# Optimization experiments

Measured on AMD Instinct MI355X. Metric: run time of the kernel, lower is better.

## Reference

```python
import jax, jax.numpy as jnp
import numpy as np

QBITS = 8  # all quant points configured to 8-bit symmetric by default


def fake_quant(v, bits=QBITS):
    """Symmetric per-tensor fake quantize/dequantize with STE-compatible form."""
    qmax = float(2 ** (bits - 1) - 1)
    scale = jnp.maximum(jnp.max(jnp.abs(v)) / qmax, 1e-8)
    q = jnp.clip(jnp.round(v / scale), -qmax - 1.0, qmax) * scale
    # straight-through estimator (identity gradient)
    return v + jax.lax.stop_gradient(q - v)


def reorder_pt_to_haste(w):
    # PyTorch gate order (r,z,n) -> Haste order (z,r,n) along leading 3H axis
    h3 = w.shape[0] // 3
    return jnp.concatenate([w[h3:2 * h3], w[:h3], w[2 * h3:]], axis=0)


def setup_inputs() -> dict:
    key = jax.random.key(0)
    ks = jax.random.split(key, 6)
    T, B, I, H = 1024, 64, 256, 256
    s = 1.0 / np.sqrt(H)
    return {
        "x": jax.random.normal(ks[0], (T, B, I), dtype=jnp.float32),
        "weight_ih": jax.random.normal(ks[1], (3 * H, I), dtype=jnp.float32) * s,
        "weight_hh": jax.random.normal(ks[2], (3 * H, H), dtype=jnp.float32) * s,
        "bias_ih": jax.random.normal(ks[3], (3 * H,), dtype=jnp.float32) * s,
        "bias_hh": jax.random.normal(ks[4], (3 * H,), dtype=jnp.float32) * s,
        "h0": jax.random.normal(ks[5], (B, H), dtype=jnp.float32),
    }


def _quant_gru(x, weight_ih, weight_hh, bias_ih, bias_hh, h0):
    T, B, I = x.shape
    H = weight_hh.shape[1]
    # Haste layout: W [I,3H], R [H,3H], gate order (z,r,n)
    W = reorder_pt_to_haste(weight_ih).T   # [I, 3H]
    R = reorder_pt_to_haste(weight_hh).T   # [H, 3H]
    bx = reorder_pt_to_haste(bias_ih)      # [3H]
    br = reorder_pt_to_haste(bias_hh)      # [3H]

    # per-tensor fake quant of inputs / weights / biases
    xq = fake_quant(x)
    Wq = fake_quant(W)
    Rq = fake_quant(R)
    bxq = fake_quant(bx)
    brq = fake_quant(br)

    # precompute Wx for all timesteps: [T,B,3H], quantized matmul output
    Wx = fake_quant(jnp.einsum('tbi,ih->tbh', xq, Wq))

    bx_z, bx_r, bx_n = bxq[:H], bxq[H:2 * H], bxq[2 * H:]
    br_z, br_r, br_n = brq[:H], brq[H:2 * H], brq[2 * H:]

    def step(h, wx_t):
        hq = fake_quant(h)
        Rh = fake_quant(hq @ Rq)           # [B, 3H]
        Rh_z, Rh_r, Rh_n = Rh[:, :H], Rh[:, H:2 * H], Rh[:, 2 * H:]
        wx_z, wx_r, wx_n = wx_t[:, :H], wx_t[:, H:2 * H], wx_t[:, 2 * H:]

        z_pre = fake_quant(wx_z + bx_z + Rh_z + br_z)
        z = fake_quant(jax.nn.sigmoid(z_pre))
        r_pre = fake_quant(wx_r + bx_r + Rh_r + br_r)
        r = fake_quant(jax.nn.sigmoid(r_pre))

        Rh_add_br = fake_quant(Rh_n + br_n)
        rRh = fake_quant(r * Rh_add_br)
        g_pre = fake_quant(wx_n + bx_n + rRh)
        g = fake_quant(jnp.tanh(g_pre))

        old_contrib = fake_quant(z * h)
        new_contrib = fake_quant((1.0 - z) * g)
        h_new = old_contrib + new_contrib
        return h_new, h_new

    h_last, output = jax.lax.scan(step, h0, Wx)  # output: [T, B, H]
    return output, h_last[None]  # h_n: [1, B, H]


def reference(x, weight_ih, weight_hh, bias_ih, bias_hh, h0):
    return _quant_gru(x, weight_ih, weight_hh, bias_ih, bias_hh, h0)
```

## Files before the change

### kernel.cpp

```cpp
#include <hip/hip_runtime.h>
#include <cstdint>
#include <cstddef>


typedef int   v4i __attribute__((ext_vector_type(4)));
typedef float v4f __attribute__((ext_vector_type(4)));

#define T_STEPS 1024
#define OUT_MAIN_FLOATS (1024*64*256)
#define WXQ_DOUT_OFF 16842752
#define NWG 8

__device__ __forceinline__ float clamp128(float x) {
  return fminf(fmaxf(x, -128.0f), 127.0f);
}
__device__ __forceinline__ int permj(int j) {
  return j < 256 ? j + 256 : (j < 512 ? j - 256 : j);
}
__device__ __forceinline__ float sigmoidf_(float x) {
  return __fdividef(1.0f, 1.0f + __expf(-x));
}
__device__ __forceinline__ float tanhf_(float x) {
  float e = __expf(-2.0f * fabsf(x));
  float t = __fdividef(1.0f - e, 1.0f + e);
  return copysignf(t, x);
}
__device__ __forceinline__ unsigned skey(float x) {
  unsigned u = __float_as_uint(x);
  return (u & 0x80000000u) ? ~u : (u | 0x80000000u);
}
__device__ __forceinline__ float sdec(unsigned k) {
  unsigned u = (k & 0x80000000u) ? (k ^ 0x80000000u) : ~k;
  return __uint_as_float(u);
}
__device__ __forceinline__ float wave_amax(float v) {
  #pragma unroll
  for (int m = 1; m <= 32; m <<= 1) v = fmaxf(v, __shfl_xor(v, m, 64));
  return v;
}

__device__ __forceinline__ unsigned dpp_wave_max(unsigned v) {
  unsigned t;
  t = (unsigned)__builtin_amdgcn_update_dpp(0, (int)v, 0x111, 0xf, 0xf, true);
  v = v > t ? v : t;
  t = (unsigned)__builtin_amdgcn_update_dpp(0, (int)v, 0x112, 0xf, 0xf, true);
  v = v > t ? v : t;
  t = (unsigned)__builtin_amdgcn_update_dpp(0, (int)v, 0x114, 0xf, 0xf, true);
  v = v > t ? v : t;
  t = (unsigned)__builtin_amdgcn_update_dpp(0, (int)v, 0x118, 0xf, 0xf, true);
  v = v > t ? v : t;
  t = (unsigned)__builtin_amdgcn_update_dpp(0, (int)v, 0x142, 0xf, 0xf, true);
  v = v > t ? v : t;
  t = (unsigned)__builtin_amdgcn_update_dpp(0, (int)v, 0x143, 0xf, 0xf, true);
  v = v > t ? v : t;
  return v;
}

__device__ __forceinline__ void bar_lgkm() {
  asm volatile("s_waitcnt lgkmcnt(0)\n\ts_barrier" ::: "memory");
  __builtin_amdgcn_sched_barrier(0);
}

__device__ __forceinline__ int poll_burst(const unsigned long long* p,
                                          unsigned tag, unsigned* val) {
  unsigned out;
  int fnd;
  unsigned long long scr;
  asm volatile(
    "s_mov_b32 %[fnd], 0\n\t"
    "global_load_dwordx2 v[80:81], %[p], off sc1\n\t"
    "global_load_dwordx2 v[82:83], %[p], off sc0 sc1\n\t"
    "global_load_dwordx2 v[84:85], %[p], off sc1\n\t"
    "global_load_dwordx2 v[86:87], %[p], off sc0 sc1\n\t"

    "s_waitcnt vmcnt(3)\n\t"
    "v_cmp_eq_u32 vcc, %[tg], v81\n\t"
    "s_xor_b64 %[scr], vcc, exec\n\t"
    "s_cbranch_scc0 F0_%=\n\t"
    "global_load_dwordx2 v[80:81], %[p], off sc1\n\t"
    "s_waitcnt vmcnt(3)\n\t"
    "v_cmp_eq_u32 vcc, %[tg], v83\n\t"
    "s_xor_b64 %[scr], vcc, exec\n\t"
    "s_cbranch_scc0 F1_%=\n\t"
    "global_load_dwordx2 v[82:83], %[p], off sc0 sc1\n\t"
    "s_waitcnt vmcnt(3)\n\t"
    "v_cmp_eq_u32 vcc, %[tg], v85\n\t"
    "s_xor_b64 %[scr], vcc, exec\n\t"
    "s_cbranch_scc0 F2_%=\n\t"
    "global_load_dwordx2 v[84:85], %[p], off sc1\n\t"
    "s_waitcnt vmcnt(3)\n\t"
    "v_cmp_eq_u32 vcc, %[tg], v87\n\t"
    "s_xor_b64 %[scr], vcc, exec\n\t"
    "s_cbranch_scc0 F3_%=\n\t"
    "global_load_dwordx2 v[86:87], %[p], off sc0 sc1\n\t"

    "s_waitcnt vmcnt(3)\n\t"
    "v_cmp_eq_u32 vcc, %[tg], v81\n\t"
    "s_xor_b64 %[scr], vcc, exec\n\t"
    "s_cbranch_scc0 F0_%=\n\t"
    "global_load_dwordx2 v[80:81], %[p], off sc1\n\t"
    "s_waitcnt vmcnt(3)\n\t"
    "v_cmp_eq_u32 vcc, %[tg], v83\n\t"
    "s_xor_b64 %[scr], vcc, exec\n\t"
    "s_cbranch_scc0 F1_%=\n\t"
    "global_load_dwordx2 v[82:83], %[p], off sc0 sc1\n\t"
    "s_waitcnt vmcnt(3)\n\t"
    "v_cmp_eq_u32 vcc, %[tg], v85\n\t"
    "s_xor_b64 %[scr], vcc, exec\n\t"
    "s_cbranch_scc0 F2_%=\n\t"
    "global_load_dwordx2 v[84:85], %[p], off sc1\n\t"
    "s_waitcnt vmcnt(3)\n\t"
    "v_cmp_eq_u32 vcc, %[tg], v87\n\t"
    "s_xor_b64 %[scr], vcc, exec\n\t"
    "s_cbranch_scc0 F3_%=\n\t"
    "global_load_dwordx2 v[86:87], %[p], off sc0 sc1\n\t"

    "s_waitcnt vmcnt(3)\n\t"
    "v_cmp_eq_u32 vcc, %[tg], v81\n\t"
    "s_xor_b64 %[scr], vcc, exec\n\t"
    "s_cbranch_scc0 F0_%=\n\t"
    "s_waitcnt vmcnt(2)\n\t"
    "v_cmp_eq_u32 vcc, %[tg], v83\n\t"
    "s_xor_b64 %[scr], vcc, exec\n\t"
    "s_cbranch_scc0 F1_%=\n\t"
    "s_waitcnt vmcnt(1)\n\t"
    "v_cmp_eq_u32 vcc, %[tg], v85\n\t"
    "s_xor_b64 %[scr], vcc, exec\n\t"
    "s_cbranch_scc0 F2_%=\n\t"
    "s_waitcnt vmcnt(0)\n\t"
    "v_cmp_eq_u32 vcc, %[tg], v87\n\t"
    "s_xor_b64 %[scr], vcc, exec\n\t"
    "s_cbranch_scc0 F3_%=\n\t"
    "v_mov_b32 %[out], 0\n\t"
    "s_branch DN_%=\n\t"

    "F0_%=:\n\t"
    "v_mov_b32 %[out], v80\n\t"
    "s_mov_b32 %[fnd], 1\n\t"
    "s_branch DN_%=\n\t"
    "F1_%=:\n\t"
    "v_mov_b32 %[out], v82\n\t"
    "s_mov_b32 %[fnd], 1\n\t"
    "s_branch DN_%=\n\t"
    "F2_%=:\n\t"
    "v_mov_b32 %[out], v84\n\t"
    "s_mov_b32 %[fnd], 1\n\t"
    "s_branch DN_%=\n\t"
    "F3_%=:\n\t"
    "v_mov_b32 %[out], v86\n\t"
    "s_mov_b32 %[fnd], 1\n\t"
    "DN_%=:\n\t"
    "s_waitcnt vmcnt(0)"
    : [out]"=&v"(out), [fnd]"=&s"(fnd), [scr]"=&s"(scr)
    : [p]"v"(p), [tg]"v"(tag)
    : "vcc", "scc", "memory",
      "v80","v81","v82","v83","v84","v85","v86","v87");
  *val = out;
  return fnd;
}

#define MFMA_I8(a, b, c) __builtin_amdgcn_mfma_i32_16x16x64_i8(a, b, c, 0, 0, 0)

__global__ void k_absmax(const float* __restrict__ p, int n4, unsigned* slot) {
  int i = blockIdx.x * blockDim.x + threadIdx.x;
  int stride = gridDim.x * blockDim.x;
  const v4f* p4 = (const v4f*)p;
  float m = 0.0f;
  for (; i < n4; i += stride) {
    v4f v = p4[i];
    m = fmaxf(m, fmaxf(fmaxf(fabsf(v[0]), fabsf(v[1])),
                       fmaxf(fabsf(v[2]), fabsf(v[3]))));
  }
  m = wave_amax(m);
  if ((threadIdx.x & 63) == 0) atomicMax(slot, __float_as_uint(m));
}

__global__ void k_frag(const float* __restrict__ src,
                       const unsigned* __restrict__ slots, int slot_idx,
                       signed char* __restrict__ dst) {
  int id = blockIdx.x * 256 + threadIdx.x;
  float s = fmaxf(__uint_as_float(slots[slot_idx]) / 127.0f, 1e-8f);
  int bq   = id & 3;
  int lane = (id >> 2) & 63;
  int kc   = (id >> 8) & 3;
  int ct   = id >> 10;
  int n = ct * 16 + (lane & 15);
  int k = kc * 64 + (lane >> 4) * 16 + bq * 4;
  const float* p = src + permj(n) * 256 + k;
  int b0 = ((int)clamp128(rintf(p[0] / s))) & 255;
  int b1 = ((int)clamp128(rintf(p[1] / s))) & 255;
  int b2 = ((int)clamp128(rintf(p[2] / s))) & 255;
  int b3 = ((int)clamp128(rintf(p[3] / s))) & 255;
  ((int*)dst)[id] = b0 | (b1 << 8) | (b2 << 16) | (b3 << 24);
}

__global__ void k_bias(const float* __restrict__ bih, const float* __restrict__ bhh,
                       const unsigned* __restrict__ slots, float* __restrict__ bqo) {
  int j = threadIdx.x;
  float s_bx = fmaxf(__uint_as_float(slots[3]) / 127.0f, 1e-8f);
  float s_br = fmaxf(__uint_as_float(slots[4]) / 127.0f, 1e-8f);
  int pr = permj(j);
  bqo[j]       = s_bx * clamp128(rintf(bih[pr] / s_bx));
  bqo[768 + j] = s_br * clamp128(rintf(bhh[pr] / s_br));
}

__global__ void k_xq(const float* __restrict__ x, const unsigned* __restrict__ slots,
                     signed char* __restrict__ xq8, int n4) {
  int i = blockIdx.x * blockDim.x + threadIdx.x;
  if (i >= n4) return;
  float s_x = fmaxf(__uint_as_float(slots[0]) / 127.0f, 1e-8f);
  v4f v = ((const v4f*)x)[i];
  int b0 = ((int)clamp128(rintf(v[0] / s_x))) & 255;
  int b1 = ((int)clamp128(rintf(v[1] / s_x))) & 255;
  int b2 = ((int)clamp128(rintf(v[2] / s_x))) & 255;
  int b3 = ((int)clamp128(rintf(v[3] / s_x))) & 255;
  ((int*)xq8)[i] = b0 | (b1 << 8) | (b2 << 16) | (b3 << 24);
}

__global__ __launch_bounds__(1024) void k_wx_i8(
    const signed char* __restrict__ xq8, const signed char* __restrict__ wf,
    unsigned* __restrict__ slots, signed char* __restrict__ wxq, int mode) {
  const int t = blockIdx.x;
  const int tid = threadIdx.x, lane = tid & 63, w = tid >> 6;
  const int cl = lane & 15, lh = lane >> 4;

  v4i Bz[4], Br[4], Bn[4];
  #pragma unroll
  for (int kc = 0; kc < 4; ++kc) {
    Bz[kc] = *(const v4i*)(wf + (((w)*4      + kc) * 64 + lane) * 16);
    Br[kc] = *(const v4i*)(wf + (((w + 16)*4 + kc) * 64 + lane) * 16);
    Bn[kc] = *(const v4i*)(wf + (((w + 32)*4 + kc) * 64 + lane) * 16);
  }
  v4i acc[3][4];
  #pragma unroll
  for (int p = 0; p < 3; ++p)
    #pragma unroll
    for (int rt = 0; rt < 4; ++rt) acc[p][rt] = (v4i){0, 0, 0, 0};

  const signed char* xr = xq8 + t * 16384;
  #pragma unroll
  for (int kc = 0; kc < 4; ++kc)
    #pragma unroll
    for (int rt = 0; rt < 4; ++rt) {
      v4i A = *(const v4i*)(xr + (rt * 16 + cl) * 256 + kc * 64 + lh * 16);
      acc[0][rt] = MFMA_I8(A, Bz[kc], acc[0][rt]);
      acc[1][rt] = MFMA_I8(A, Br[kc], acc[1][rt]);
      acc[2][rt] = MFMA_I8(A, Bn[kc], acc[2][rt]);
    }

  if (mode == 0) {
    int mm = 0;
    #pragma unroll
    for (int p = 0; p < 3; ++p)
      #pragma unroll
      for (int rt = 0; rt < 4; ++rt)
        #pragma unroll
        for (int rg = 0; rg < 4; ++rg) mm = max(mm, abs(acc[p][rt][rg]));
    #pragma unroll
    for (int m = 1; m <= 32; m <<= 1) mm = max(mm, __shfl_xor(mm, m, 64));
    if (lane == 0) atomicMax((int*)(slots + 5), mm);
  } else {
    int islot = *(const int*)(slots + 5);
    float maxMf = (float)islot;
    float s_x = fmaxf(__uint_as_float(slots[0]) / 127.0f, 1e-8f);
    float s_W = fmaxf(__uint_as_float(slots[1]) / 127.0f, 1e-8f);
    float s_xW = s_x * s_W;
    float s_wx = fmaxf(s_xW * maxMf / 127.0f, 1e-8f);
    #pragma unroll
    for (int p = 0; p < 3; ++p)
      #pragma unroll
      for (int rt = 0; rt < 4; ++rt) {
        int dw = 0;
        #pragma unroll
        for (int rg = 0; rg < 4; ++rg) {
          float qf = clamp128(rintf((s_xW * (float)acc[p][rt][rg]) / s_wx));
          dw |= (((int)qf) & 255) << (rg * 8);
        }
        ((int*)wxq)[t * 12288 + p * 4096 + rt * 1024 + w * 64 + lh * 16 + cl] = dw;
      }
  }
}

template <int NCH>
__device__ __forceinline__ void xchg(unsigned* keys, unsigned tag,
    unsigned (*lred)[8], unsigned long long* gslot, int wg, int tid, int lane) {
  const int rset = tag % 3;
  #pragma unroll
  for (int c = 0; c < NCH; ++c) keys[c] = dpp_wave_max(keys[c]);
  if (lane == 63) {
    #pragma unroll
    for (int c = 0; c < NCH; ++c) atomicMax(&lred[rset][c], keys[c]);
  }
  bar_lgkm();
  const int par = tag & 1;
  if (tid < NCH) {
    unsigned long long v =
        ((unsigned long long)tag << 32) | (unsigned long long)lred[rset][tid];
    __hip_atomic_store(&gslot[(par * NWG + wg) * 8 + tid], v,
                       __ATOMIC_RELAXED, __HIP_MEMORY_SCOPE_AGENT);
  } else if (tid == 32) {
    int ns = rset + 1; if (ns == 3) ns = 0;
    #pragma unroll
    for (int c = 0; c < 8; ++c) lred[ns][c] = 0u;
  } else if (tid >= 64 && tid < 64 + (NWG - 1) * NCH) {
    int idx = tid - 64;
    int owi = idx / NCH;
    int c = idx - owi * NCH;
    int ow = owi + (owi >= wg ? 1 : 0);
    unsigned long long* p = &gslot[(par * NWG + ow) * 8 + c];
    unsigned val;
    for (;;) {
      if (poll_burst(p, tag, &val)) break;
      unsigned long long v =
          __hip_atomic_load(p, __ATOMIC_RELAXED, __HIP_MEMORY_SCOPE_AGENT);
      if ((unsigned)(v >> 32) == tag) { val = (unsigned)v; break; }
    }
    atomicMax(&lred[rset][c], val);
  }
  bar_lgkm();
  #pragma unroll
  for (int c = 0; c < NCH; ++c) keys[c] = lred[rset][c];
}

__global__ __launch_bounds__(512, 1) void k_recur8(
    const signed char* __restrict__ wxq, const signed char* __restrict__ brf,
    const float* __restrict__ bq, const unsigned* __restrict__ slots,
    const float* __restrict__ h0p, float* __restrict__ out,
    unsigned long long* __restrict__ gslot) {
  __shared__ signed char ah[16 * 272];
  __shared__ int zs[8 * 256];
  __shared__ int rs_[8 * 256];
  __shared__ int ns_[8 * 256];
  __shared__ unsigned lred[3][8];

  const int tid = threadIdx.x;
  const int lane = tid & 63;
  const int w = tid >> 6;
  const int cl = lane & 15;
  const int lh = lane >> 4;
  const int wg = blockIdx.x;
  const int j = tid & 255;
  const int rblk = tid >> 8;

  if (tid < 24) ((unsigned*)lred)[tid] = 0u;
  for (int i = tid; i < 1088; i += 512) ((int*)ah)[i] = 0;

  float s_x = fmaxf(__uint_as_float(slots[0]) / 127.0f, 1e-8f);
  float s_W = fmaxf(__uint_as_float(slots[1]) / 127.0f, 1e-8f);
  float s_R = fmaxf(__uint_as_float(slots[2]) / 127.0f, 1e-8f);
  float maxM0 = (float)(*(const int*)(slots + 5));
  float s_wx = fmaxf(s_x * s_W * maxM0 / 127.0f, 1e-8f);

  float bxz = bq[j], bxr = bq[j + 256], bxn = bq[j + 512];
  float brz = bq[768 + j], brr = bq[1024 + j], brn = bq[1280 + j];

  v4i Bz[2][4], Br[2][4], Bn[2][4];
  #pragma unroll
  for (int cg = 0; cg < 2; ++cg) {
    int ct = w * 2 + cg;
    #pragma unroll
    for (int kc = 0; kc < 4; ++kc) {
      Bz[cg][kc] = *(const v4i*)(brf + ((ct * 4        + kc) * 64 + lane) * 16);
      Br[cg][kc] = *(const v4i*)(brf + (((ct + 16) * 4 + kc) * 64 + lane) * 16);
      Bn[cg][kc] = *(const v4i*)(brf + (((ct + 32) * 4 + kc) * 64 + lane) * 16);
    }
  }

  float h[4];
  #pragma unroll
  for (int rg = 0; rg < 4; ++rg)
    h[rg] = h0p[(wg * 8 + rblk * 4 + rg) * 256 + j];

  __syncthreads();

  unsigned tag = 1;
  float sh;
  {
    float m = fmaxf(fmaxf(fabsf(h[0]), fabsf(h[1])),
                    fmaxf(fabsf(h[2]), fabsf(h[3])));
    unsigned kk[1] = {__float_as_uint(m)};
    xchg<1>(kk, tag++, lred, gslot, wg, tid, lane);
    sh = fmaxf(__uint_as_float(kk[0]) / 127.0f, 1e-8f);
    float ish = 1.0f / sh;
    #pragma unroll
    for (int rg = 0; rg < 4; ++rg)
      ah[(rblk * 4 + rg) * 272 + j] = (signed char)(int)rintf(h[rg] * ish);
    bar_lgkm();
  }

  const int rt_ = wg >> 1;
  const int lhb = ((wg & 1) << 1) | rblk;
  const int widx0 = rt_ * 1024 + (j >> 4) * 64 + lhb * 16 + (j & 15);

  for (int t = 0; t < T_STEPS; ++t) {
    const int* wxi = (const int*)wxq + (size_t)t * 12288 + widx0;
    int wvz = wxi[0];
    int wvr = wxi[4096];
    int wvn = wxi[8192];

    v4i aZ[2] = {(v4i){0,0,0,0}, (v4i){0,0,0,0}};
    v4i aR[2] = {(v4i){0,0,0,0}, (v4i){0,0,0,0}};
    v4i aN[2] = {(v4i){0,0,0,0}, (v4i){0,0,0,0}};
    #pragma unroll
    for (int kc = 0; kc < 4; ++kc) {
      v4i A = *(const v4i*)(ah + cl * 272 + kc * 64 + lh * 16);
      #pragma unroll
      for (int cg = 0; cg < 2; ++cg) {
        aZ[cg] = MFMA_I8(A, Bz[cg][kc], aZ[cg]);
        aR[cg] = MFMA_I8(A, Br[cg][kc], aR[cg]);
        aN[cg] = MFMA_I8(A, Bn[cg][kc], aN[cg]);
      }
    }

    if (lane < 32) {
      #pragma unroll
      for (int cg = 0; cg < 2; ++cg) {
        int jj = (w * 2 + cg) * 16 + cl;
        #pragma unroll
        for (int rg = 0; rg < 4; ++rg) {
          int row = lh * 4 + rg;
          zs[row * 256 + jj] = aZ[cg][rg];
          rs_[row * 256 + jj] = aR[cg][rg];
          ns_[row * 256 + jj] = aN[cg][rg];
        }
      }
    }

    int mm = 0;
    #pragma unroll
    for (int cg = 0; cg < 2; ++cg)
      #pragma unroll
      for (int rg = 0; rg < 4; ++rg)
        mm = max(mm, max(abs(aZ[cg][rg]),
                         max(abs(aR[cg][rg]), abs(aN[cg][rg]))));
    unsigned kk[5];
    kk[0] = (unsigned)mm;
    xchg<1>(kk, tag++, lred, gslot, wg, tid, lane);
    float maxMf = (float)(int)kk[0];
    float s_Rh = fmaxf(sh * s_R * maxMf / 127.0f, 1e-8f);
    float fRh = (sh * s_R) / s_Rh;

    float zp[4], rp[4], nb[4];
    float az = 0.0f, ar = 0.0f, an = 0.0f;
    float mzs = -3.402823466e38f, mrs = -3.402823466e38f;
    #pragma unroll
    for (int rg = 0; rg < 4; ++rg) {
      int row = rblk * 4 + rg;
      float Rz = s_Rh * rintf((float)zs[row * 256 + j] * fRh);
      float Rr = s_Rh * rintf((float)rs_[row * 256 + j] * fRh);
      float Rn = s_Rh * rintf((float)ns_[row * 256 + j] * fRh);
      float wz = s_wx * (float)((signed char)(wvz >> (rg * 8)));
      float wr = s_wx * (float)((signed char)(wvr >> (rg * 8)));
      float a1 = ((wz + bxz) + Rz) + brz;
      float a2 = ((wr + bxr) + Rr) + brr;
      float a3 = Rn + brn;
      zp[rg] = a1; rp[rg] = a2; nb[rg] = a3;
      az = fmaxf(az, fabsf(a1)); ar = fmaxf(ar, fabsf(a2));
      an = fmaxf(an, fabsf(a3));
      mzs = fmaxf(mzs, a1); mrs = fmaxf(mrs, a2);
    }
    kk[0] = __float_as_uint(az); kk[1] = __float_as_uint(ar);
    kk[2] = __float_as_uint(an); kk[3] = skey(mzs); kk[4] = skey(mrs);
    xchg<5>(kk, tag++, lred, gslot, wg, tid, lane);
    float s1 = fmaxf(__uint_as_float(kk[0]) / 127.0f, 1e-8f), i1 = 1.0f / s1;
    float s2 = fmaxf(__uint_as_float(kk[1]) / 127.0f, 1e-8f), i2 = 1.0f / s2;
    float s3 = fmaxf(__uint_as_float(kk[2]) / 127.0f, 1e-8f), i3 = 1.0f / s3;
    float zq_max = s1 * rintf(sdec(kk[3]) * i1);
    float rq_max = s2 * rintf(sdec(kk[4]) * i2);
    float s4 = fmaxf(sigmoidf_(zq_max) / 127.0f, 1e-8f), i4 = 1.0f / s4;
    float s5 = fmaxf(sigmoidf_(rq_max) / 127.0f, 1e-8f), i5 = 1.0f / s5;

    float zf[4], rr_[4];
    float m6 = 0.0f;
    #pragma unroll
    for (int rg = 0; rg < 4; ++rg) {
      float zq = s1 * rintf(zp[rg] * i1);
      float rq = s2 * rintf(rp[rg] * i2);
      float zv = sigmoidf_(zq);
      float rv = sigmoidf_(rq);
      zf[rg] = s4 * rintf(zv * i4);
      float rq2 = s5 * rintf(rv * i5);
      float nbq = s3 * rintf(nb[rg] * i3);
      float rr = rq2 * nbq;
      rr_[rg] = rr;
      m6 = fmaxf(m6, fabsf(rr));
    }
    kk[0] = __float_as_uint(m6);
    xchg<1>(kk, tag++, lred, gslot, wg, tid, lane);
    float s6 = fmaxf(__uint_as_float(kk[0]) / 127.0f, 1e-8f), i6 = 1.0f / s6;

    float gp[4];
    float m7 = 0.0f;
    #pragma unroll
    for (int rg = 0; rg < 4; ++rg) {
      float rrq = s6 * rintf(rr_[rg] * i6);
      float wn = s_wx * (float)((signed char)(wvn >> (rg * 8)));
      float g = (wn + bxn) + rrq;
      gp[rg] = g;
      m7 = fmaxf(m7, fabsf(g));
    }
    kk[0] = __float_as_uint(m7);
    xchg<1>(kk, tag++, lred, gslot, wg, tid, lane);
    float m7g = __uint_as_float(kk[0]);
    float s7 = fmaxf(m7g / 127.0f, 1e-8f), i7 = 1.0f / s7;
    float gq_max = s7 * rintf(m7g * i7);
    float s8 = fmaxf(tanhf_(gq_max) / 127.0f, 1e-8f), i8v = 1.0f / s8;

    float ov[4], nv[4];
    float mo = 0.0f, mn = 0.0f;
    #pragma unroll
    for (int rg = 0; rg < 4; ++rg) {
      float gpq = s7 * rintf(gp[rg] * i7);
      float gv = tanhf_(gpq);
      float gq = s8 * rintf(gv * i8v);
      float o = zf[rg] * h[rg];
      float n = (1.0f - zf[rg]) * gq;
      ov[rg] = o; nv[rg] = n;
      mo = fmaxf(mo, fabsf(o)); mn = fmaxf(mn, fabsf(n));
    }
    kk[0] = __float_as_uint(mo); kk[1] = __float_as_uint(mn);
    xchg<2>(kk, tag++, lred, gslot, wg, tid, lane);
    float s9  = fmaxf(__uint_as_float(kk[0]) / 127.0f, 1e-8f), i9  = 1.0f / s9;
    float s10 = fmaxf(__uint_as_float(kk[1]) / 127.0f, 1e-8f), i10 = 1.0f / s10;

    float mh = 0.0f;
    #pragma unroll
    for (int rg = 0; rg < 4; ++rg) {
      float oq = s9  * rintf(ov[rg] * i9);
      float nq = s10 * rintf(nv[rg] * i10);
      float hn = oq + nq;
      h[rg] = hn;
      mh = fmaxf(mh, fabsf(hn));
      out[t * 16384 + (wg * 8 + rblk * 4 + rg) * 256 + j] = hn;
    }
    kk[0] = __float_as_uint(mh);
    xchg<1>(kk, tag++, lred, gslot, wg, tid, lane);
    sh = fmaxf(__uint_as_float(kk[0]) / 127.0f, 1e-8f);
    float ish = 1.0f / sh;
    #pragma unroll
    for (int rg = 0; rg < 4; ++rg)
      ah[(rblk * 4 + rg) * 272 + j] = (signed char)(int)rintf(h[rg] * ish);
    bar_lgkm();
  }

  #pragma unroll
  for (int rg = 0; rg < 4; ++rg)
    out[OUT_MAIN_FLOATS + (wg * 8 + rblk * 4 + rg) * 256 + j] = h[rg];
}

extern "C" void kernel_launch(void* const* d_in, const int* in_sizes, int n_in,
                              void* d_out, int out_size, void* d_ws, size_t ws_size,
                              hipStream_t stream) {
  const float* x   = (const float*)d_in[0];
  const float* wih = (const float*)d_in[1];
  const float* whh = (const float*)d_in[2];
  const float* bih = (const float*)d_in[3];
  const float* bhh = (const float*)d_in[4];
  const float* h0  = (const float*)d_in[5];
  float* out = (float*)d_out;

  unsigned* slots = (unsigned*)d_ws;
  unsigned long long* gslot = (unsigned long long*)((char*)d_ws + 512);
  float* bq       = (float*)((char*)d_ws + 4096);
  signed char* F  = (signed char*)d_ws + 10240;

  signed char* wxq = (signed char*)d_out + WXQ_DOUT_OFF;
  signed char* xq8 = (signed char*)d_out;

  hipMemsetAsync(d_ws, 0, 4096, stream);

  k_absmax<<<dim3(1024), dim3(256), 0, stream>>>(x,   16777216 / 4, slots + 0);
  k_absmax<<<dim3(96),   dim3(256), 0, stream>>>(wih, 196608 / 4,   slots + 1);
  k_absmax<<<dim3(96),   dim3(256), 0, stream>>>(whh, 196608 / 4,   slots + 2);
  k_absmax<<<dim3(1),    dim3(256), 0, stream>>>(bih, 768 / 4,      slots + 3);
  k_absmax<<<dim3(1),    dim3(256), 0, stream>>>(bhh, 768 / 4,      slots + 4);

  k_frag<<<dim3(192), dim3(256), 0, stream>>>(wih, slots, 1, F);
  k_bias<<<dim3(1), dim3(768), 0, stream>>>(bih, bhh, slots, bq);
  k_xq<<<dim3(16384), dim3(256), 0, stream>>>(x, slots, xq8, 4194304);

  k_wx_i8<<<dim3(1024), dim3(1024), 0, stream>>>(xq8, F, slots, wxq, 0);
  k_wx_i8<<<dim3(1024), dim3(1024), 0, stream>>>(xq8, F, slots, wxq, 1);

  k_frag<<<dim3(192), dim3(256), 0, stream>>>(whh, slots, 2, F);

  k_recur8<<<dim3(NWG), dim3(512), 0, stream>>>(wxq, F, bq, slots, h0, out,
                                                gslot);
}
```

Before: 12.70 ms.

## Replace first block barrier in cross-workgroup max exchange with last-arriver counter

```diff
diff --git a/kernel.cpp b/kernel.cpp
--- a/kernel.cpp
+++ b/kernel.cpp
@@ -283,26 +283,42 @@
 
 template <int NCH>
 __device__ __forceinline__ void xchg(unsigned* keys, unsigned tag,
-    unsigned (*lred)[8], unsigned long long* gslot, int wg, int tid, int lane) {
+    unsigned (*lred)[8], unsigned* lredw, unsigned* cnt,
+    unsigned long long* gslot, int wg, int tid, int lane, int w) {
   const int rset = tag % 3;
+  const int par = tag & 1;
   #pragma unroll
   for (int c = 0; c < NCH; ++c) keys[c] = dpp_wave_max(keys[c]);
+  int old = -1;
   if (lane == 63) {
     #pragma unroll
-    for (int c = 0; c < NCH; ++c) atomicMax(&lred[rset][c], keys[c]);
-  }
-  bar_lgkm();
-  const int par = tag & 1;
-  if (tid < NCH) {
-    unsigned long long v =
-        ((unsigned long long)tag << 32) | (unsigned long long)lred[rset][tid];
-    __hip_atomic_store(&gslot[(par * NWG + wg) * 8 + tid], v,
-                       __ATOMIC_RELAXED, __HIP_MEMORY_SCOPE_AGENT);
-  } else if (tid == 32) {
+    for (int c = 0; c < NCH; ++c) lredw[c * 8 + w] = keys[c];
+    asm volatile("s_waitcnt lgkmcnt(0)" ::: "memory");
+    old = (int)atomicAdd(&cnt[rset], 1u);
+  }
+  if (old == 7) {
+    #pragma unroll
+    for (int c = 0; c < NCH; ++c) {
+      unsigned M = lredw[c * 8 + 0];
+      #pragma unroll
+      for (int ww = 1; ww < 8; ++ww) {
+        unsigned t2 = lredw[c * 8 + ww];
+        M = M > t2 ? M : t2;
+      }
+      unsigned long long v =
+          ((unsigned long long)tag << 32) | (unsigned long long)M;
+      __hip_atomic_store(&gslot[(par * NWG + wg) * 8 + c], v,
+                         __ATOMIC_RELAXED, __HIP_MEMORY_SCOPE_AGENT);
+      atomicMax(&lred[rset][c], M);
+    }
+  }
+  if (tid == 32) {
     int ns = rset + 1; if (ns == 3) ns = 0;
     #pragma unroll
     for (int c = 0; c < 8; ++c) lred[ns][c] = 0u;
-  } else if (tid >= 64 && tid < 64 + (NWG - 1) * NCH) {
+    cnt[ns] = 0u;
+  }
+  if (tid >= 64 && tid < 64 + (NWG - 1) * NCH) {
     int idx = tid - 64;
     int owi = idx / NCH;
     int c = idx - owi * NCH;
@@ -332,6 +348,8 @@
   __shared__ int rs_[8 * 256];
   __shared__ int ns_[8 * 256];
   __shared__ unsigned lred[3][8];
+  __shared__ unsigned lredw[64];
+  __shared__ unsigned cnt[3];
 
   const int tid = threadIdx.x;
   const int lane = tid & 63;
@@ -343,6 +361,7 @@
   const int rblk = tid >> 8;
 
   if (tid < 24) ((unsigned*)lred)[tid] = 0u;
+  if (tid >= 24 && tid < 27) cnt[tid - 24] = 0u;
   for (int i = tid; i < 1088; i += 512) ((int*)ah)[i] = 0;
 
   float s_x = fmaxf(__uint_as_float(slots[0]) / 127.0f, 1e-8f);
@@ -379,7 +398,7 @@
     float m = fmaxf(fmaxf(fabsf(h[0]), fabsf(h[1])),
                     fmaxf(fabsf(h[2]), fabsf(h[3])));
     unsigned kk[1] = {__float_as_uint(m)};
-    xchg<1>(kk, tag++, lred, gslot, wg, tid, lane);
+    xchg<1>(kk, tag++, lred, lredw, cnt, gslot, wg, tid, lane, w);
     sh = fmaxf(__uint_as_float(kk[0]) / 127.0f, 1e-8f);
     float ish = 1.0f / sh;
     #pragma unroll
@@ -435,7 +454,7 @@
                          max(abs(aR[cg][rg]), abs(aN[cg][rg]))));
     unsigned kk[5];
     kk[0] = (unsigned)mm;
-    xchg<1>(kk, tag++, lred, gslot, wg, tid, lane);
+    xchg<1>(kk, tag++, lred, lredw, cnt, gslot, wg, tid, lane, w);
     float maxMf = (float)(int)kk[0];
     float s_Rh = fmaxf(sh * s_R * maxMf / 127.0f, 1e-8f);
     float fRh = (sh * s_R) / s_Rh;
@@ -461,7 +480,7 @@
     }
     kk[0] = __float_as_uint(az); kk[1] = __float_as_uint(ar);
     kk[2] = __float_as_uint(an); kk[3] = skey(mzs); kk[4] = skey(mrs);
-    xchg<5>(kk, tag++, lred, gslot, wg, tid, lane);
+    xchg<5>(kk, tag++, lred, lredw, cnt, gslot, wg, tid, lane, w);
     float s1 = fmaxf(__uint_as_float(kk[0]) / 127.0f, 1e-8f), i1 = 1.0f / s1;
     float s2 = fmaxf(__uint_as_float(kk[1]) / 127.0f, 1e-8f), i2 = 1.0f / s2;
     float s3 = fmaxf(__uint_as_float(kk[2]) / 127.0f, 1e-8f), i3 = 1.0f / s3;
@@ -486,7 +505,7 @@
       m6 = fmaxf(m6, fabsf(rr));
     }
     kk[0] = __float_as_uint(m6);
-    xchg<1>(kk, tag++, lred, gslot, wg, tid, lane);
+    xchg<1>(kk, tag++, lred, lredw, cnt, gslot, wg, tid, lane, w);
     float s6 = fmaxf(__uint_as_float(kk[0]) / 127.0f, 1e-8f), i6 = 1.0f / s6;
 
     float gp[4];
@@ -500,7 +519,7 @@
       m7 = fmaxf(m7, fabsf(g));
     }
     kk[0] = __float_as_uint(m7);
-    xchg<1>(kk, tag++, lred, gslot, wg, tid, lane);
+    xchg<1>(kk, tag++, lred, lredw, cnt, gslot, wg, tid, lane, w);
     float m7g = __uint_as_float(kk[0]);
     float s7 = fmaxf(m7g / 127.0f, 1e-8f), i7 = 1.0f / s7;
     float gq_max = s7 * rintf(m7g * i7);
@@ -519,7 +538,7 @@
       mo = fmaxf(mo, fabsf(o)); mn = fmaxf(mn, fabsf(n));
     }
     kk[0] = __float_as_uint(mo); kk[1] = __float_as_uint(mn);
-    xchg<2>(kk, tag++, lred, gslot, wg, tid, lane);
+    xchg<2>(kk, tag++, lred, lredw, cnt, gslot, wg, tid, lane, w);
     float s9  = fmaxf(__uint_as_float(kk[0]) / 127.0f, 1e-8f), i9  = 1.0f / s9;
     float s10 = fmaxf(__uint_as_float(kk[1]) / 127.0f, 1e-8f), i10 = 1.0f / s10;
 
@@ -534,7 +553,7 @@
       out[t * 16384 + (wg * 8 + rblk * 4 + rg) * 256 + j] = hn;
     }
     kk[0] = __float_as_uint(mh);
-    xchg<1>(kk, tag++, lred, gslot, wg, tid, lane);
+    xchg<1>(kk, tag++, lred, lredw, cnt, gslot, wg, tid, lane, w);
     sh = fmaxf(__uint_as_float(kk[0]) / 127.0f, 1e-8f);
     float ish = 1.0f / sh;
     #pragma unroll
```

After: 14.09 ms. +11.0%, slower.

## Double recurrence block to 1024 threads, one MFMA column tile per wave

Applied to the files above, without the earlier changes.

```diff
diff --git a/kernel.cpp b/kernel.cpp
--- a/kernel.cpp
+++ b/kernel.cpp
@@ -322,7 +322,7 @@
   for (int c = 0; c < NCH; ++c) keys[c] = lred[rset][c];
 }
 
-__global__ __launch_bounds__(512, 1) void k_recur8(
+__global__ __launch_bounds__(1024, 1) void k_recur8(
     const signed char* __restrict__ wxq, const signed char* __restrict__ brf,
     const float* __restrict__ bq, const unsigned* __restrict__ slots,
     const float* __restrict__ h0p, float* __restrict__ out,
@@ -343,7 +343,7 @@
   const int rblk = tid >> 8;
 
   if (tid < 24) ((unsigned*)lred)[tid] = 0u;
-  for (int i = tid; i < 1088; i += 512) ((int*)ah)[i] = 0;
+  for (int i = tid; i < 1088; i += 1024) ((int*)ah)[i] = 0;
 
   float s_x = fmaxf(__uint_as_float(slots[0]) / 127.0f, 1e-8f);
   float s_W = fmaxf(__uint_as_float(slots[1]) / 127.0f, 1e-8f);
@@ -354,43 +354,39 @@
   float bxz = bq[j], bxr = bq[j + 256], bxn = bq[j + 512];
   float brz = bq[768 + j], brr = bq[1024 + j], brn = bq[1280 + j];
 
-  v4i Bz[2][4], Br[2][4], Bn[2][4];
-  #pragma unroll
-  for (int cg = 0; cg < 2; ++cg) {
-    int ct = w * 2 + cg;
-    #pragma unroll
-    for (int kc = 0; kc < 4; ++kc) {
-      Bz[cg][kc] = *(const v4i*)(brf + ((ct * 4        + kc) * 64 + lane) * 16);
-      Br[cg][kc] = *(const v4i*)(brf + (((ct + 16) * 4 + kc) * 64 + lane) * 16);
-      Bn[cg][kc] = *(const v4i*)(brf + (((ct + 32) * 4 + kc) * 64 + lane) * 16);
-    }
-  }
-
-  float h[4];
-  #pragma unroll
-  for (int rg = 0; rg < 4; ++rg)
-    h[rg] = h0p[(wg * 8 + rblk * 4 + rg) * 256 + j];
+  v4i Bz[4], Br[4], Bn[4];
+  #pragma unroll
+  for (int kc = 0; kc < 4; ++kc) {
+    Bz[kc] = *(const v4i*)(brf + ((w * 4        + kc) * 64 + lane) * 16);
+    Br[kc] = *(const v4i*)(brf + (((w + 16) * 4 + kc) * 64 + lane) * 16);
+    Bn[kc] = *(const v4i*)(brf + (((w + 32) * 4 + kc) * 64 + lane) * 16);
+  }
+
+  float h[2];
+  #pragma unroll
+  for (int s = 0; s < 2; ++s)
+    h[s] = h0p[(wg * 8 + rblk * 2 + s) * 256 + j];
 
   __syncthreads();
 
   unsigned tag = 1;
   float sh;
   {
-    float m = fmaxf(fmaxf(fabsf(h[0]), fabsf(h[1])),
-                    fmaxf(fabsf(h[2]), fabsf(h[3])));
+    float m = fmaxf(fabsf(h[0]), fabsf(h[1]));
     unsigned kk[1] = {__float_as_uint(m)};
     xchg<1>(kk, tag++, lred, gslot, wg, tid, lane);
     sh = fmaxf(__uint_as_float(kk[0]) / 127.0f, 1e-8f);
     float ish = 1.0f / sh;
     #pragma unroll
-    for (int rg = 0; rg < 4; ++rg)
-      ah[(rblk * 4 + rg) * 272 + j] = (signed char)(int)rintf(h[rg] * ish);
+    for (int s = 0; s < 2; ++s)
+      ah[(rblk * 2 + s) * 272 + j] = (signed char)(int)rintf(h[s] * ish);
     bar_lgkm();
   }
 
-  const int rt_ = wg >> 1;
-  const int lhb = ((wg & 1) << 1) | rblk;
-  const int widx0 = rt_ * 1024 + (j >> 4) * 64 + lhb * 16 + (j & 15);
+  const int widx0 = (wg >> 1) * 1024 +
+                    (((wg << 1) | (rblk >> 1)) & 3) * 16 +
+                    (j >> 4) * 64 + (j & 15);
+  const int bb = (rblk & 1) * 2;
 
   for (int t = 0; t < T_STEPS; ++t) {
     const int* wxi = (const int*)wxq + (size_t)t * 12288 + widx0;
@@ -398,41 +394,30 @@
     int wvr = wxi[4096];
     int wvn = wxi[8192];
 
-    v4i aZ[2] = {(v4i){0,0,0,0}, (v4i){0,0,0,0}};
-    v4i aR[2] = {(v4i){0,0,0,0}, (v4i){0,0,0,0}};
-    v4i aN[2] = {(v4i){0,0,0,0}, (v4i){0,0,0,0}};
+    v4i aZ = {0,0,0,0}, aR = {0,0,0,0}, aN = {0,0,0,0};
     #pragma unroll
     for (int kc = 0; kc < 4; ++kc) {
       v4i A = *(const v4i*)(ah + cl * 272 + kc * 64 + lh * 16);
+      aZ = MFMA_I8(A, Bz[kc], aZ);
+      aR = MFMA_I8(A, Br[kc], aR);
+      aN = MFMA_I8(A, Bn[kc], aN);
+    }
+
+    if (lane < 32) {
+      int jj = w * 16 + cl;
       #pragma unroll
-      for (int cg = 0; cg < 2; ++cg) {
-        aZ[cg] = MFMA_I8(A, Bz[cg][kc], aZ[cg]);
-        aR[cg] = MFMA_I8(A, Br[cg][kc], aR[cg]);
-        aN[cg] = MFMA_I8(A, Bn[cg][kc], aN[cg]);
+      for (int rg = 0; rg < 4; ++rg) {
+        int row = lh * 4 + rg;
+        zs[row * 256 + jj] = aZ[rg];
+        rs_[row * 256 + jj] = aR[rg];
+        ns_[row * 256 + jj] = aN[rg];
       }
     }
 
-    if (lane < 32) {
-      #pragma unroll
-      for (int cg = 0; cg < 2; ++cg) {
-        int jj = (w * 2 + cg) * 16 + cl;
-        #pragma unroll
-        for (int rg = 0; rg < 4; ++rg) {
-          int row = lh * 4 + rg;
-          zs[row * 256 + jj] = aZ[cg][rg];
-          rs_[row * 256 + jj] = aR[cg][rg];
-          ns_[row * 256 + jj] = aN[cg][rg];
-        }
-      }
-    }
-
     int mm = 0;
     #pragma unroll
-    for (int cg = 0; cg < 2; ++cg)
-      #pragma unroll
-      for (int rg = 0; rg < 4; ++rg)
-        mm = max(mm, max(abs(aZ[cg][rg]),
-                         max(abs(aR[cg][rg]), abs(aN[cg][rg]))));
+    for (int rg = 0; rg < 4; ++rg)
+      mm = max(mm, max(abs(aZ[rg]), max(abs(aR[rg]), abs(aN[rg]))));
     unsigned kk[5];
     kk[0] = (unsigned)mm;
     xchg<1>(kk, tag++, lred, gslot, wg, tid, lane);
@@ -440,21 +425,21 @@
     float s_Rh = fmaxf(sh * s_R * maxMf / 127.0f, 1e-8f);
     float fRh = (sh * s_R) / s_Rh;
 
-    float zp[4], rp[4], nb[4];
+    float zp[2], rp[2], nb[2];
     float az = 0.0f, ar = 0.0f, an = 0.0f;
     float mzs = -3.402823466e38f, mrs = -3.402823466e38f;
     #pragma unroll
-    for (int rg = 0; rg < 4; ++rg) {
-      int row = rblk * 4 + rg;
+    for (int s = 0; s < 2; ++s) {
+      int row = rblk * 2 + s;
       float Rz = s_Rh * rintf((float)zs[row * 256 + j] * fRh);
       float Rr = s_Rh * rintf((float)rs_[row * 256 + j] * fRh);
       float Rn = s_Rh * rintf((float)ns_[row * 256 + j] * fRh);
-      float wz = s_wx * (float)((signed char)(wvz >> (rg * 8)));
-      float wr = s_wx * (float)((signed char)(wvr >> (rg * 8)));
+      float wz = s_wx * (float)((signed char)(wvz >> ((bb + s) * 8)));
+      float wr = s_wx * (float)((signed char)(wvr >> ((bb + s) * 8)));
       float a1 = ((wz + bxz) + Rz) + brz;
       float a2 = ((wr + bxr) + Rr) + brr;
       float a3 = Rn + brn;
-      zp[rg] = a1; rp[rg] = a2; nb[rg] = a3;
+      zp[s] = a1; rp[s] = a2; nb[s] = a3;
       az = fmaxf(az, fabsf(a1)); ar = fmaxf(ar, fabsf(a2));
       an = fmaxf(an, fabsf(a3));
       mzs = fmaxf(mzs, a1); mrs = fmaxf(mrs, a2);
@@ -470,33 +455,33 @@
     float s4 = fmaxf(sigmoidf_(zq_max) / 127.0f, 1e-8f), i4 = 1.0f / s4;
     float s5 = fmaxf(sigmoidf_(rq_max) / 127.0f, 1e-8f), i5 = 1.0f / s5;
 
-    float zf[4], rr_[4];
+    float zf[2], rr_[2];
     float m6 = 0.0f;
     #pragma unroll
-    for (int rg = 0; rg < 4; ++rg) {
-      float zq = s1 * rintf(zp[rg] * i1);
-      float rq = s2 * rintf(rp[rg] * i2);
+    for (int s = 0; s < 2; ++s) {
+      float zq = s1 * rintf(zp[s] * i1);
+      float rq = s2 * rintf(rp[s] * i2);
       float zv = sigmoidf_(zq);
       float rv = sigmoidf_(rq);
-      zf[rg] = s4 * rintf(zv * i4);
+      zf[s] = s4 * rintf(zv * i4);
       float rq2 = s5 * rintf(rv * i5);
-      float nbq = s3 * rintf(nb[rg] * i3);
+      float nbq = s3 * rintf(nb[s] * i3);
       float rr = rq2 * nbq;
-      rr_[rg] = rr;
+      rr_[s] = rr;
       m6 = fmaxf(m6, fabsf(rr));
     }
     kk[0] = __float_as_uint(m6);
     xchg<1>(kk, tag++, lred, gslot, wg, tid, lane);
     float s6 = fmaxf(__uint_as_float(kk[0]) / 127.0f, 1e-8f), i6 = 1.0f / s6;
 
-    float gp[4];
+    float gp[2];
     float m7 = 0.0f;
     #pragma unroll
-    for (int rg = 0; rg < 4; ++rg) {
-      float rrq = s6 * rintf(rr_[rg] * i6);
-      float wn = s_wx * (float)((signed char)(wvn >> (rg * 8)));
+    for (int s = 0; s < 2; ++s) {
+      float rrq = s6 * rintf(rr_[s] * i6);
+      float wn = s_wx * (float)((signed char)(wvn >> ((bb + s) * 8)));
       float g = (wn + bxn) + rrq;
-      gp[rg] = g;
+      gp[s] = g;
       m7 = fmaxf(m7, fabsf(g));
     }
     kk[0] = __float_as_uint(m7);
@@ -506,16 +491,16 @@
     float gq_max = s7 * rintf(m7g * i7);
     float s8 = fmaxf(tanhf_(gq_max) / 127.0f, 1e-8f), i8v = 1.0f / s8;
 
-    float ov[4], nv[4];
+    float ov[2], nv[2];
     float mo = 0.0f, mn = 0.0f;
     #pragma unroll
-    for (int rg = 0; rg < 4; ++rg) {
-      float gpq = s7 * rintf(gp[rg] * i7);
+    for (int s = 0; s < 2; ++s) {
+      float gpq = s7 * rintf(gp[s] * i7);
       float gv = tanhf_(gpq);
       float gq = s8 * rintf(gv * i8v);
-      float o = zf[rg] * h[rg];
-      float n = (1.0f - zf[rg]) * gq;
-      ov[rg] = o; nv[rg] = n;
+      float o = zf[s] * h[s];
+      float n = (1.0f - zf[s]) * gq;
+      ov[s] = o; nv[s] = n;
       mo = fmaxf(mo, fabsf(o)); mn = fmaxf(mn, fabsf(n));
     }
     kk[0] = __float_as_uint(mo); kk[1] = __float_as_uint(mn);
@@ -525,27 +510,27 @@
 
     float mh = 0.0f;
     #pragma unroll
-    for (int rg = 0; rg < 4; ++rg) {
-      float oq = s9  * rintf(ov[rg] * i9);
-      float nq = s10 * rintf(nv[rg] * i10);
+    for (int s = 0; s < 2; ++s) {
+      float oq = s9  * rintf(ov[s] * i9);
+      float nq = s10 * rintf(nv[s] * i10);
       float hn = oq + nq;
-      h[rg] = hn;
+      h[s] = hn;
       mh = fmaxf(mh, fabsf(hn));
-      out[t * 16384 + (wg * 8 + rblk * 4 + rg) * 256 + j] = hn;
+      out[t * 16384 + (wg * 8 + rblk * 2 + s) * 256 + j] = hn;
     }
     kk[0] = __float_as_uint(mh);
     xchg<1>(kk, tag++, lred, gslot, wg, tid, lane);
     sh = fmaxf(__uint_as_float(kk[0]) / 127.0f, 1e-8f);
     float ish = 1.0f / sh;
     #pragma unroll
-    for (int rg = 0; rg < 4; ++rg)
-      ah[(rblk * 4 + rg) * 272 + j] = (signed char)(int)rintf(h[rg] * ish);
+    for (int s = 0; s < 2; ++s)
+      ah[(rblk * 2 + s) * 272 + j] = (signed char)(int)rintf(h[s] * ish);
     bar_lgkm();
   }
 
   #pragma unroll
-  for (int rg = 0; rg < 4; ++rg)
-    out[OUT_MAIN_FLOATS + (wg * 8 + rblk * 4 + rg) * 256 + j] = h[rg];
+  for (int s = 0; s < 2; ++s)
+    out[OUT_MAIN_FLOATS + (wg * 8 + rblk * 2 + s) * 256 + j] = h[s];
 }
 
 extern "C" void kernel_launch(void* const* d_in, const int* in_sizes, int n_in,
@@ -584,6 +569,6 @@
 
   k_frag<<<dim3(192), dim3(256), 0, stream>>>(whh, slots, 2, F);
 
-  k_recur8<<<dim3(NWG), dim3(512), 0, stream>>>(wxq, F, bq, slots, h0, out,
-                                                gslot);
-}
+  k_recur8<<<dim3(NWG), dim3(1024), 0, stream>>>(wxq, F, bq, slots, h0, out,
+                                                 gslot);
+}
```

Measured after the change: 14.03 ms. +10.5%, slower.
